# Kernel tuning notes

Hardware: AMD Instinct MI355X
Metric: run time of the kernel (lower is better)

Reference implementation:

```python
import jax, jax.numpy as jnp
import numpy as np

HID, QK_NOPE, QK_ROPE, Q_LR, KV_LR, H, V_DIM = 2048, 128, 64, 768, 512, 16, 128
QK_HEAD = QK_NOPE + QK_ROPE
THETA = 10000.0
EPS = 1e-5


def _layernorm(x, g, b):
    mu = jnp.mean(x, axis=-1, keepdims=True)
    var = jnp.mean(jnp.square(x - mu), axis=-1, keepdims=True)
    return (x - mu) * jax.lax.rsqrt(var + EPS) * g + b


def _rotate_half(x):
    x1, x2 = jnp.split(x, 2, axis=-1)
    return jnp.concatenate([-x2, x1], axis=-1)


def setup_inputs() -> dict:
    key = jax.random.key(0)
    ks = jax.random.split(key, 6)
    s = 0.02
    return {
        "hidden_state": jax.random.normal(ks[0], (2, 4096, HID), dtype=jnp.float32),
        "w_qa": jax.random.normal(ks[1], (Q_LR, HID), dtype=jnp.float32) * s,
        "b_qa": jnp.zeros((Q_LR,), jnp.float32),
        "g_qa_ln": jnp.ones((Q_LR,), jnp.float32),
        "b_qa_ln": jnp.zeros((Q_LR,), jnp.float32),
        "w_qb": jax.random.normal(ks[2], (H * QK_HEAD, Q_LR), dtype=jnp.float32) * s,
        "b_qb": jnp.zeros((H * QK_HEAD,), jnp.float32),
        "w_kva": jax.random.normal(ks[3], (KV_LR + QK_ROPE, HID), dtype=jnp.float32) * s,
        "b_kva": jnp.zeros((KV_LR + QK_ROPE,), jnp.float32),
        "g_kva_ln": jnp.ones((KV_LR,), jnp.float32),
        "b_kva_ln": jnp.zeros((KV_LR,), jnp.float32),
        "w_kvb": jax.random.normal(ks[4], (H * (QK_NOPE + V_DIM), KV_LR), dtype=jnp.float32) * s,
        "b_kvb": jnp.zeros((H * (QK_NOPE + V_DIM),), jnp.float32),
    }


def reference(hidden_state, w_qa, b_qa, g_qa_ln, b_qa_ln, w_qb, b_qb,
              w_kva, b_kva, g_kva_ln, b_kva_ln, w_kvb, b_kvb):
    B, S, _ = hidden_state.shape
    # ----- Q path: low-rank down-proj -> LN -> up-proj -----
    q_c = hidden_state @ w_qa.T + b_qa                      # [B,S,Q_LR]
    q_c = _layernorm(q_c, g_qa_ln, b_qa_ln)
    q = (q_c @ w_qb.T + b_qb).reshape(B, S, H, QK_HEAD).transpose(0, 2, 1, 3)  # [B,H,S,QK_HEAD]
    q_nope, q_rope = q[..., :QK_NOPE], q[..., QK_NOPE:]
    # ----- KV path -----
    kv_c = hidden_state @ w_kva.T + b_kva                   # [B,S,KV_LR+ROPE]
    kv_lr, k_rope = kv_c[..., :KV_LR], kv_c[..., KV_LR:]
    kv_lr = _layernorm(kv_lr, g_kva_ln, b_kva_ln)
    kv = (kv_lr @ w_kvb.T + b_kvb).reshape(B, S, H, QK_NOPE + V_DIM).transpose(0, 2, 1, 3)
    k_nope, v = kv[..., :QK_NOPE], kv[..., QK_NOPE:]
    # ----- RoPE on the rope slice only -----
    inv_freq = 1.0 / THETA ** (jnp.arange(0, QK_ROPE, 2, dtype=jnp.float32) / QK_ROPE)
    freq = jnp.arange(S, dtype=jnp.float32)[:, None] * inv_freq[None, :]   # [S, ROPE/2]
    cos = jnp.concatenate([jnp.cos(freq), jnp.cos(freq)], axis=-1)[None, None]  # [1,1,S,ROPE]
    sin = jnp.concatenate([jnp.sin(freq), jnp.sin(freq)], axis=-1)[None, None]
    k_rope = k_rope[:, None]                                # [B,1,S,ROPE]
    q_rot = q_rope * cos + _rotate_half(q_rope) * sin       # [B,H,S,ROPE]
    k_rot = k_rope * cos + _rotate_half(k_rope) * sin       # [B,1,S,ROPE]
    k_rot = jnp.broadcast_to(k_rot, (B, H, S, QK_ROPE))
    q_full = jnp.concatenate([q_nope, q_rot], axis=-1)      # [B,H,S,QK_HEAD]
    k_full = jnp.concatenate([k_nope, k_rot], axis=-1)      # [B,H,S,QK_HEAD]
    # original forward stops after building q,k,v; return them concatenated
    return jnp.concatenate([q_full, k_full, v], axis=-1)    # [B,H,S,2*QK_HEAD+V_DIM]
```

## Files before the change

kernel.cpp:

```cpp
#include <hip/hip_runtime.h>

typedef unsigned short u16;
typedef __bf16 bf16x8 __attribute__((ext_vector_type(8)));
typedef float f32x4 __attribute__((ext_vector_type(4)));

#define FENCE() asm volatile("" ::: "memory")
#define BARRIER()                      \
  do {                                 \
    FENCE();                           \
    __builtin_amdgcn_s_barrier();      \
    FENCE();                           \
  } while (0)


__device__ __forceinline__ u16 f2bf(float f) {
  unsigned u = __float_as_uint(f);
  u += 0x7fffu + ((u >> 16) & 1u);
  return (u16)(u >> 16);
}

__device__ __forceinline__ ushort4 f2bf4(float4 v) {
  return make_ushort4(f2bf(v.x), f2bf(v.y), f2bf(v.z), f2bf(v.w));
}

__device__ __forceinline__ void load_lds16(const void* g, void* l) {
  __builtin_amdgcn_global_load_lds(
      (const __attribute__((address_space(1))) void*)g,
      (__attribute__((address_space(3))) void*)l, 16, 0, 0);
}

__device__ __forceinline__ void conv_seg(const float* __restrict__ s,
                                         u16* __restrict__ d, int n4,
                                         int g, int stride) {
  const float4* s4 = (const float4*)s;
  ushort4* d4 = (ushort4*)d;
  for (int i = g; i < n4; i += stride) {
    float4 v = s4[i];
    d4[i] = make_ushort4(f2bf(v.x), f2bf(v.y), f2bf(v.z), f2bf(v.w));
  }
}


__global__ __launch_bounds__(256) void prep(
    const float* __restrict__ hid, const float* __restrict__ wqa,
    const float* __restrict__ wkva, const float* __restrict__ wqb,
    const float* __restrict__ wkvb, const float* __restrict__ bqa,
    const float* __restrict__ bkva, u16* __restrict__ hid_b,
    u16* __restrict__ wab_b, u16* __restrict__ wqb_b,
    u16* __restrict__ wkvb_b, float* __restrict__ bias_ab,
    float* __restrict__ cosT, float* __restrict__ sinT) {
  int g = blockIdx.x * 256 + threadIdx.x;
  int stride = gridDim.x * 256;
  conv_seg(hid, hid_b, 4194304, g, stride);
  conv_seg(wqa, wab_b, 393216, g, stride);
  conv_seg(wkva, wab_b + 768 * 2048, 294912, g, stride);
  conv_seg(wqb, wqb_b, 589824, g, stride);
  conv_seg(wkvb, wkvb_b, 524288, g, stride);
  if (g < 1344) bias_ab[g] = (g < 768) ? bqa[g] : bkva[g - 768];
  for (int idx = g; idx < 131072; idx += stride) {
    int s = idx >> 5, i = idx & 31;
    float inv = powf(10000.f, -(float)i / 32.f);
    float f = (float)s * inv;
    float sv, cv;
    sincosf(f, &sv, &cv);
    cosT[idx] = cv;
    sinT[idx] = sv;
  }
}


template <int WHICH>
__global__ __launch_bounds__(256, 2) void gemm_k(
    const u16* __restrict__ A0, const u16* __restrict__ B0,
    const float* __restrict__ bias0, float* __restrict__ C0,
    const u16* __restrict__ qA, const u16* __restrict__ qB,
    const float* __restrict__ qb, const u16* __restrict__ kA,
    const u16* __restrict__ kB, const float* __restrict__ kb,
    float* __restrict__ out, const float* __restrict__ cosT,
    const float* __restrict__ sinT) {
  __shared__ __align__(16) u16 smem[2 * 128 * 64];
  u16* sA = smem;
  u16* sB = smem + 128 * 64;
  const int tid = threadIdx.x;
  const int lane = tid & 63;
  const int wave = tid >> 6;
  const int wm = (wave >> 1) * 64;
  const int wn = (wave & 1) * 64;
  const int lane15 = lane & 15;
  const int quad = lane >> 4;
  const int mTile = blockIdx.x * 128;

  const u16* A;
  const u16* B;
  const float* bias;
  int K, nTile, mode;
  if (WHICH == 0) {
    A = A0; B = B0; bias = bias0; K = 2048; nTile = blockIdx.y * 128; mode = 0;
  } else if (blockIdx.y < 24) {
    A = qA; B = qB; bias = qb; K = 768; nTile = blockIdx.y * 128; mode = 1;
  } else {
    A = kA; B = kB; bias = kb; K = 512; nTile = (blockIdx.y - 24) * 128;
    mode = 2;
  }

  f32x4 acc[4][4] = {};

  const int nStages = K >> 6;
  for (int ks = 0; ks < nStages; ++ks) {
    const int k0 = ks << 6;
    if (ks) __syncthreads();
#pragma unroll
    for (int i = 0; i < 4; ++i) {
      int nu = i * 256 + tid;
      int rr = nu >> 3, u = nu & 7;
      int ul = u ^ (rr & 7);
      load_lds16(A + (size_t)(mTile + rr) * K + (k0 + ul * 8),
                 &sA[(i * 256 + (wave << 6)) * 8]);
    }
#pragma unroll
    for (int i = 0; i < 4; ++i) {
      int nu = i * 256 + tid;
      int rr = nu >> 3, u = nu & 7;
      int ul = u ^ (rr & 7);
      int brow = nTile + rr;
      if (WHICH == 0 && brow >= 1344) brow = 1343;
      load_lds16(B + (size_t)brow * K + (k0 + ul * 8),
                 &sB[(i * 256 + (wave << 6)) * 8]);
    }
    __syncthreads();
#pragma unroll
    for (int kk = 0; kk < 2; ++kk) {
      bf16x8 af[4], bfv[4];
#pragma unroll
      for (int mi = 0; mi < 4; ++mi) {
        int r = wm + mi * 16 + lane15;
        int u = (kk * 4 + quad) ^ (r & 7);
        af[mi] = *(const bf16x8*)&sA[(r * 8 + u) * 8];
      }
#pragma unroll
      for (int ni = 0; ni < 4; ++ni) {
        int r = wn + ni * 16 + lane15;
        int u = (kk * 4 + quad) ^ (r & 7);
        bfv[ni] = *(const bf16x8*)&sB[(r * 8 + u) * 8];
      }
#pragma unroll
      for (int mi = 0; mi < 4; ++mi)
#pragma unroll
        for (int ni = 0; ni < 4; ++ni)
          acc[mi][ni] = __builtin_amdgcn_mfma_f32_16x16x32_bf16(
              af[mi], bfv[ni], acc[mi][ni], 0, 0, 0);
    }
  }

  const int colW = nTile + wn;
  float bv[4];
#pragma unroll
  for (int ni = 0; ni < 4; ++ni) {
    int col = colW + ni * 16 + lane15;
    if (WHICH == 0)
      bv[ni] = (col < 1344) ? bias[col] : 0.f;
    else
      bv[ni] = bias[col];
  }

  int h = 0, ch0 = 0;
  if (mode == 1) {
    h = colW / 192;
    ch0 = colW % 192;
  } else if (mode == 2) {
    int jb = colW & 255;
    h = colW >> 8;
    ch0 = (jb < 128) ? (192 + jb) : (256 + jb);
  }
  const bool ropeTile = (mode == 1) && (ch0 == 128);

  __syncthreads();
  float* lw = (float*)smem + wave * (16 * 68);
  const int hi = lane15 >> 2, l3 = lane15 & 3;

#pragma unroll
  for (int mi = 0; mi < 4; ++mi) {
    f32x4 v[4];
#pragma unroll
    for (int ni = 0; ni < 4; ++ni)
#pragma unroll
      for (int rg = 0; rg < 4; ++rg) v[ni][rg] = acc[mi][ni][rg] + bv[ni];

    if (ropeTile) {
      int rowB = mTile + wm + mi * 16 + quad * 4;
#pragma unroll
      for (int rg = 0; rg < 4; ++rg) {
        int ss = (rowB + rg) & 4095;
#pragma unroll
        for (int ni = 0; ni < 2; ++ni) {
          int i = ni * 16 + lane15;
          float cv = cosT[ss * 32 + i], sv = sinT[ss * 32 + i];
          float x1 = v[ni][rg], x2 = v[ni + 2][rg];
          v[ni][rg] = x1 * cv - x2 * sv;
          v[ni + 2][rg] = x2 * cv + x1 * sv;
        }
      }
    }

    if (mi) asm volatile("s_waitcnt lgkmcnt(0)" ::: "memory");
#pragma unroll
    for (int ni = 0; ni < 4; ++ni) {
      int su = (4 * ni + hi) ^ quad;
#pragma unroll
      for (int rg = 0; rg < 4; ++rg)
        lw[68 * (quad * 4 + rg) + 4 * su + l3] = v[ni][rg];
    }
    asm volatile("s_waitcnt lgkmcnt(0)" ::: "memory");
#pragma unroll
    for (int j = 0; j < 4; ++j) {
      int rr = 4 * j + quad;
      int su = lane15 ^ j;
      float4 o = *(const float4*)&lw[68 * rr + 4 * su];
      int row = mTile + wm + mi * 16 + rr;
      if (mode == 0) {
        if (colW + 4 * lane15 < 1344)
          *(float4*)(C0 + (size_t)row * 1344 + colW + 4 * lane15) = o;
      } else {
        int bb = row >> 12, ss = row & 4095;
        size_t ob =
            ((size_t)((bb * 16 + h) * 4096 + ss)) * 512 + ch0 + 4 * lane15;
        *(float4*)(out + ob) = o;
      }
    }
  }
}

__global__ __launch_bounds__(512, 2) void gemm256(
    const u16* __restrict__ A, const u16* __restrict__ B,
    const float* __restrict__ bias, float* __restrict__ out) {
  __shared__ __align__(16) u16 smem[4 * 256 * 64];
  const int tid = threadIdx.x;
  const int lane = tid & 63;
  const int wave = tid >> 6;
  const int wm = (wave >> 2) * 128;
  const int wn = (wave & 3) * 64;
  const int lane15 = lane & 15;
  const int quad = lane >> 4;
  const int mTile = blockIdx.x * 256;
  const int nTile = blockIdx.y * 256;

  u16* const sA0 = smem;
  u16* const sB0 = smem + 2 * 16384;

#define STAGE8(kt, c)                                                         \
  do {                                                                        \
    u16* dA = sA0 + (c) * 16384;                                              \
    u16* dB = sB0 + (c) * 16384;                                              \
    _Pragma("unroll") for (int i = 0; i < 4; ++i) {                           \
      int g = i * 512 + tid;                                                  \
      int rr = g >> 3, ul = (g & 7) ^ (rr & 7);                               \
      load_lds16(A + (size_t)(mTile + rr) * 512 + (kt) * 64 + ul * 8,         \
                 dA + (i * 512 + (wave << 6)) * 8);                           \
    }                                                                         \
    _Pragma("unroll") for (int i = 0; i < 4; ++i) {                           \
      int g = i * 512 + tid;                                                  \
      int rr = g >> 3, ul = (g & 7) ^ (rr & 7);                               \
      load_lds16(B + (size_t)(nTile + rr) * 512 + (kt) * 64 + ul * 8,         \
                 dB + (i * 512 + (wave << 6)) * 8);                           \
    }                                                                         \
  } while (0)

  f32x4 acc[8][4] = {};

  STAGE8(0, 0);
  for (int t = 0; t < 8; ++t) {
    const int c = t & 1;
    const u16* sAc = sA0 + c * 16384;
    const u16* sBc = sB0 + c * 16384;
    if (t < 7) {
      STAGE8(t + 1, c ^ 1);
      asm volatile("s_waitcnt vmcnt(8)" ::: "memory");
    } else {
      asm volatile("s_waitcnt vmcnt(0)" ::: "memory");
    }
    BARRIER();
#pragma unroll
    for (int ph = 0; ph < 4; ++ph) {
      const int mh = ph >> 1, nh = ph & 1;
      bf16x8 af[4][2], bfv[2][2];
#pragma unroll
      for (int mi = 0; mi < 4; ++mi) {
        int r = wm + mh * 64 + mi * 16 + lane15;
#pragma unroll
        for (int kk = 0; kk < 2; ++kk) {
          int u = (kk * 4 + quad) ^ (r & 7);
          af[mi][kk] = *(const bf16x8*)&sAc[(r * 8 + u) * 8];
        }
      }
#pragma unroll
      for (int ni = 0; ni < 2; ++ni) {
        int rb = wn + nh * 32 + ni * 16 + lane15;
#pragma unroll
        for (int kk = 0; kk < 2; ++kk) {
          int u = (kk * 4 + quad) ^ (rb & 7);
          bfv[ni][kk] = *(const bf16x8*)&sBc[(rb * 8 + u) * 8];
        }
      }
      BARRIER();
      __builtin_amdgcn_s_setprio(1);
#pragma unroll
      for (int mi = 0; mi < 4; ++mi)
#pragma unroll
        for (int ni = 0; ni < 2; ++ni)
#pragma unroll
          for (int kk = 0; kk < 2; ++kk)
            acc[mh * 4 + mi][nh * 2 + ni] =
                __builtin_amdgcn_mfma_f32_16x16x32_bf16(
                    af[mi][kk], bfv[ni][kk], acc[mh * 4 + mi][nh * 2 + ni],
                    0, 0, 0);
      __builtin_amdgcn_s_setprio(0);
      BARRIER();
    }
  }
#undef STAGE8

  const int colW = nTile + wn;
  float bv[4];
#pragma unroll
  for (int ni = 0; ni < 4; ++ni) bv[ni] = bias[colW + ni * 16 + lane15];
  const int h = colW >> 8;
  const int jb = colW & 255;
  const int ch0 = (jb < 128) ? (192 + jb) : (256 + jb);

  float* lw = (float*)smem + wave * (16 * 68);
  const int hi = lane15 >> 2, l3 = lane15 & 3;

#pragma unroll
  for (int mi = 0; mi < 8; ++mi) {
    f32x4 v[4];
#pragma unroll
    for (int ni = 0; ni < 4; ++ni)
#pragma unroll
      for (int rg = 0; rg < 4; ++rg) v[ni][rg] = acc[mi][ni][rg] + bv[ni];

    if (mi) asm volatile("s_waitcnt lgkmcnt(0)" ::: "memory");
#pragma unroll
    for (int ni = 0; ni < 4; ++ni) {
      int su = (4 * ni + hi) ^ quad;
#pragma unroll
      for (int rg = 0; rg < 4; ++rg)
        lw[68 * (quad * 4 + rg) + 4 * su + l3] = v[ni][rg];
    }
    asm volatile("s_waitcnt lgkmcnt(0)" ::: "memory");
#pragma unroll
    for (int j = 0; j < 4; ++j) {
      int rr = 4 * j + quad;
      int su = lane15 ^ j;
      float4 o = *(const float4*)&lw[68 * rr + 4 * su];
      int row = mTile + wm + mi * 16 + rr;
      int bb = row >> 12, ss = row & 4095;
      size_t ob =
          ((size_t)((bb * 16 + h) * 4096 + ss)) * 512 + ch0 + 4 * lane15;
      *(float4*)(out + ob) = o;
    }
  }
}


__global__ __launch_bounds__(256) void ln_rot(
    const float* __restrict__ qkvc, const float* __restrict__ g_q,
    const float* __restrict__ b_q, const float* __restrict__ g_kv,
    const float* __restrict__ b_kv, u16* __restrict__ q_ln,
    u16* __restrict__ kv_ln, const float* __restrict__ cosT,
    const float* __restrict__ sinT, float* __restrict__ out) {
  __shared__ float red[4][4];
  __shared__ __align__(16) float rot[64];
  const int tid = threadIdx.x;
  const int t = blockIdx.x;
  const int bb = t >> 12, ss = t & 4095;
  const float4* p4 = (const float4*)(qkvc + (size_t)t * 1344);

  float4 a = p4[tid];
  float4 b = make_float4(0.f, 0.f, 0.f, 0.f);
  if (tid < 80) b = p4[256 + tid];

  float sa = a.x + a.y + a.z + a.w;
  float sqa = a.x * a.x + a.y * a.y + a.z * a.z + a.w * a.w;
  float qs = 0.f, qq = 0.f, ks = 0.f, kq = 0.f;
  if (tid < 192) { qs = sa; qq = sqa; } else { ks = sa; kq = sqa; }
  if (tid < 64) {
    ks += b.x + b.y + b.z + b.w;
    kq += b.x * b.x + b.y * b.y + b.z * b.z + b.w * b.w;
  }
#pragma unroll
  for (int off = 32; off > 0; off >>= 1) {
    qs += __shfl_down(qs, off, 64);
    qq += __shfl_down(qq, off, 64);
    ks += __shfl_down(ks, off, 64);
    kq += __shfl_down(kq, off, 64);
  }
  const int lane = tid & 63, wave = tid >> 6;
  if (lane == 0) {
    red[wave][0] = qs; red[wave][1] = qq;
    red[wave][2] = ks; red[wave][3] = kq;
  }
  __syncthreads();
  qs = red[0][0] + red[1][0] + red[2][0] + red[3][0];
  qq = red[0][1] + red[1][1] + red[2][1] + red[3][1];
  ks = red[0][2] + red[1][2] + red[2][2] + red[3][2];
  kq = red[0][3] + red[1][3] + red[2][3] + red[3][3];
  const float muq = qs * (1.f / 768.f);
  const float invq = rsqrtf(qq * (1.f / 768.f) - muq * muq + 1e-5f);
  const float muk = ks * (1.f / 512.f);
  const float invk = rsqrtf(kq * (1.f / 512.f) - muk * muk + 1e-5f);

  if (tid < 192) {
    float4 g = ((const float4*)g_q)[tid];
    float4 be = ((const float4*)b_q)[tid];
    float4 o = make_float4((a.x - muq) * invq * g.x + be.x,
                           (a.y - muq) * invq * g.y + be.y,
                           (a.z - muq) * invq * g.z + be.z,
                           (a.w - muq) * invq * g.w + be.w);
    ((ushort4*)(q_ln + (size_t)t * 768))[tid] = f2bf4(o);
  } else {
    int j = tid - 192;
    float4 g = ((const float4*)g_kv)[j];
    float4 be = ((const float4*)b_kv)[j];
    float4 o = make_float4((a.x - muk) * invk * g.x + be.x,
                           (a.y - muk) * invk * g.y + be.y,
                           (a.z - muk) * invk * g.z + be.z,
                           (a.w - muk) * invk * g.w + be.w);
    ((ushort4*)(kv_ln + (size_t)t * 512))[j] = f2bf4(o);
  }
  if (tid < 64) {
    int j = 64 + tid;
    float4 g = ((const float4*)g_kv)[j];
    float4 be = ((const float4*)b_kv)[j];
    float4 o = make_float4((b.x - muk) * invk * g.x + be.x,
                           (b.y - muk) * invk * g.y + be.y,
                           (b.z - muk) * invk * g.z + be.z,
                           (b.w - muk) * invk * g.w + be.w);
    ((ushort4*)(kv_ln + (size_t)t * 512))[j] = f2bf4(o);
  }
  if (tid < 32) {
    const float* p = qkvc + (size_t)t * 1344;
    float k1 = p[1280 + tid], k2 = p[1312 + tid];
    float cv = cosT[ss * 32 + tid], sv = sinT[ss * 32 + tid];
    rot[tid] = k1 * cv - k2 * sv;
    rot[tid + 32] = k2 * cv + k1 * sv;
  }
  __syncthreads();
  {
    int hh = tid >> 4, c4 = tid & 15;
    float4 o = ((const float4*)rot)[c4];
    *(float4*)(out + ((size_t)((bb * 16 + hh) * 4096 + ss)) * 512 + 320 +
               4 * c4) = o;
  }
}


extern "C" void kernel_launch(void* const* d_in, const int* in_sizes, int n_in,
                              void* d_out, int out_size, void* d_ws,
                              size_t ws_size, hipStream_t stream) {
  const float* hidden = (const float*)d_in[0];
  const float* w_qa = (const float*)d_in[1];
  const float* b_qa = (const float*)d_in[2];
  const float* g_qa_ln = (const float*)d_in[3];
  const float* b_qa_ln = (const float*)d_in[4];
  const float* w_qb = (const float*)d_in[5];
  const float* b_qb = (const float*)d_in[6];
  const float* w_kva = (const float*)d_in[7];
  const float* b_kva = (const float*)d_in[8];
  const float* g_kva_ln = (const float*)d_in[9];
  const float* b_kva_ln = (const float*)d_in[10];
  const float* w_kvb = (const float*)d_in[11];
  const float* b_kvb = (const float*)d_in[12];
  float* out = (float*)d_out;

  char* ws = (char*)d_ws;
  u16* hid_bf = (u16*)ws;   ws += (size_t)16777216 * 2;
  u16* wab_bf = (u16*)ws;   ws += (size_t)1344 * 2048 * 2;
  u16* wqb_bf = (u16*)ws;   ws += (size_t)2359296 * 2;
  u16* wkvb_bf = (u16*)ws;  ws += (size_t)2097152 * 2;
  float* qkvc = (float*)ws; ws += (size_t)8192 * 1344 * 4;
  u16* q_ln = (u16*)ws;     ws += (size_t)6291456 * 2;
  u16* kv_ln = (u16*)ws;    ws += (size_t)4194304 * 2;
  float* cosT = (float*)ws; ws += (size_t)131072 * 4;
  float* sinT = (float*)ws; ws += (size_t)131072 * 4;
  float* bias_ab = (float*)ws; ws += (size_t)2048 * 4;

  prep<<<dim3(1024), dim3(256), 0, stream>>>(
      hidden, w_qa, w_kva, w_qb, w_kvb, b_qa, b_kva, hid_bf, wab_bf, wqb_bf,
      wkvb_bf, bias_ab, cosT, sinT);
  gemm_k<0><<<dim3(64, 11), dim3(256), 0, stream>>>(
      hid_bf, wab_bf, bias_ab, qkvc, nullptr, nullptr, nullptr, nullptr,
      nullptr, nullptr, nullptr, cosT, sinT);
  ln_rot<<<dim3(8192), dim3(256), 0, stream>>>(qkvc, g_qa_ln, b_qa_ln,
                                               g_kva_ln, b_kva_ln, q_ln, kv_ln,
                                               cosT, sinT, out);
  gemm_k<1><<<dim3(64, 24), dim3(256), 0, stream>>>(
      nullptr, nullptr, nullptr, nullptr, q_ln, wqb_bf, b_qb, nullptr, nullptr,
      nullptr, out, cosT, sinT);
  gemm256<<<dim3(32, 16), dim3(512), 0, stream>>>(kv_ln, wkvb_bf, b_kvb, out);
}
```

Before: 480.3 us.

## Restructure KV up-projection GEMM into triple-buffered K=32 pipeline

The 256x256 KV GEMM now uses 16 k-steps of width 32 with a three-stage LDS ring instead of 8 steps of width 64 double-buffered. Loads for step j+2 are interleaved between the two MFMA halves, and each step has one barrier instead of eight barriers per tile. Shared memory drops to 96 KB and launch bounds allow one block per CU, trading occupancy for deeper prefetch and fewer synchronisations. The swizzle changes to match the narrower 4-chunk rows.

Result: slower. 490.8 us (+2.2%).

```diff
diff --git a/kernel.cpp b/kernel.cpp
--- a/kernel.cpp
+++ b/kernel.cpp
@@ -230,10 +230,10 @@
   }
 }
 
-__global__ __launch_bounds__(512, 2) void gemm256(
+__global__ __launch_bounds__(512, 1) void gemm256kv(
     const u16* __restrict__ A, const u16* __restrict__ B,
     const float* __restrict__ bias, float* __restrict__ out) {
-  __shared__ __align__(16) u16 smem[4 * 256 * 64];
+  __shared__ __align__(16) u16 smem[6 * 8192];
   const int tid = threadIdx.x;
   const int lane = tid & 63;
   const int wave = tid >> 6;
@@ -244,80 +244,77 @@
   const int mTile = blockIdx.x * 256;
   const int nTile = blockIdx.y * 256;
 
-  u16* const sA0 = smem;
-  u16* const sB0 = smem + 2 * 16384;
-
-#define STAGE8(kt, c)                                                         \
+#define STG(SRC, rowBase, kt, dstBase)                                        \
   do {                                                                        \
-    u16* dA = sA0 + (c) * 16384;                                              \
-    u16* dB = sB0 + (c) * 16384;                                              \
-    _Pragma("unroll") for (int i = 0; i < 4; ++i) {                           \
-      int g = i * 512 + tid;                                                  \
-      int rr = g >> 3, ul = (g & 7) ^ (rr & 7);                               \
-      load_lds16(A + (size_t)(mTile + rr) * 512 + (kt) * 64 + ul * 8,         \
-                 dA + (i * 512 + (wave << 6)) * 8);                           \
-    }                                                                         \
-    _Pragma("unroll") for (int i = 0; i < 4; ++i) {                           \
-      int g = i * 512 + tid;                                                  \
-      int rr = g >> 3, ul = (g & 7) ^ (rr & 7);                               \
-      load_lds16(B + (size_t)(nTile + rr) * 512 + (kt) * 64 + ul * 8,         \
-                 dB + (i * 512 + (wave << 6)) * 8);                           \
+    _Pragma("unroll") for (int l = 0; l < 2; ++l) {                           \
+      int g = l * 512 + tid;                                                  \
+      int rr = g >> 2;                                                        \
+      int ul = (g & 3) ^ ((rr >> 1) & 3);                                     \
+      load_lds16(SRC + (size_t)((rowBase) + rr) * 512 + (kt) * 32 + ul * 8,   \
+                 (dstBase) + (size_t)(l * 512 + (wave << 6)) * 8);            \
     }                                                                         \
   } while (0)
 
   f32x4 acc[8][4] = {};
 
-  STAGE8(0, 0);
-  for (int t = 0; t < 8; ++t) {
-    const int c = t & 1;
-    const u16* sAc = sA0 + c * 16384;
-    const u16* sBc = sB0 + c * 16384;
-    if (t < 7) {
-      STAGE8(t + 1, c ^ 1);
-      asm volatile("s_waitcnt vmcnt(8)" ::: "memory");
-    } else {
+  STG(A, mTile, 0, smem);
+  STG(B, nTile, 0, smem + 3 * 8192);
+  STG(A, mTile, 1, smem + 8192);
+  STG(B, nTile, 1, smem + 3 * 8192 + 8192);
+  asm volatile("s_waitcnt vmcnt(4)" ::: "memory");
+  BARRIER();
+
+  int s = 0;
+  for (int j = 0; j < 16; ++j) {
+    const u16* sAc = smem + s * 8192;
+    const u16* sBc = smem + (3 + s) * 8192;
+    int s2 = s + 2; if (s2 >= 3) s2 -= 3;
+
+    bf16x8 af[4], bfv[4];
+#pragma unroll
+    for (int mi = 0; mi < 4; ++mi) {
+      int r = wm + mi * 16 + lane15;
+      af[mi] = *(const bf16x8*)&sAc[(r * 4 + (quad ^ ((r >> 1) & 3))) * 8];
+    }
+#pragma unroll
+    for (int ni = 0; ni < 4; ++ni) {
+      int rb = wn + ni * 16 + lane15;
+      bfv[ni] = *(const bf16x8*)&sBc[(rb * 4 + (quad ^ ((rb >> 1) & 3))) * 8];
+    }
+    if (j < 14) STG(A, mTile, j + 2, smem + s2 * 8192);
+    __builtin_amdgcn_s_setprio(1);
+#pragma unroll
+    for (int mi = 0; mi < 4; ++mi)
+#pragma unroll
+      for (int ni = 0; ni < 4; ++ni)
+        acc[mi][ni] = __builtin_amdgcn_mfma_f32_16x16x32_bf16(
+            af[mi], bfv[ni], acc[mi][ni], 0, 0, 0);
+    __builtin_amdgcn_s_setprio(0);
+
+    bf16x8 af2[4];
+#pragma unroll
+    for (int mi = 0; mi < 4; ++mi) {
+      int r = wm + 64 + mi * 16 + lane15;
+      af2[mi] = *(const bf16x8*)&sAc[(r * 4 + (quad ^ ((r >> 1) & 3))) * 8];
+    }
+    if (j < 14) STG(B, nTile, j + 2, smem + (3 + s2) * 8192);
+    __builtin_amdgcn_s_setprio(1);
+#pragma unroll
+    for (int mi = 0; mi < 4; ++mi)
+#pragma unroll
+      for (int ni = 0; ni < 4; ++ni)
+        acc[4 + mi][ni] = __builtin_amdgcn_mfma_f32_16x16x32_bf16(
+            af2[mi], bfv[ni], acc[4 + mi][ni], 0, 0, 0);
+    __builtin_amdgcn_s_setprio(0);
+
+    if (j < 14)
+      asm volatile("s_waitcnt vmcnt(4)" ::: "memory");
+    else if (j == 14)
       asm volatile("s_waitcnt vmcnt(0)" ::: "memory");
-    }
     BARRIER();
-#pragma unroll
-    for (int ph = 0; ph < 4; ++ph) {
-      const int mh = ph >> 1, nh = ph & 1;
-      bf16x8 af[4][2], bfv[2][2];
-#pragma unroll
-      for (int mi = 0; mi < 4; ++mi) {
-        int r = wm + mh * 64 + mi * 16 + lane15;
-#pragma unroll
-        for (int kk = 0; kk < 2; ++kk) {
-          int u = (kk * 4 + quad) ^ (r & 7);
-          af[mi][kk] = *(const bf16x8*)&sAc[(r * 8 + u) * 8];
-        }
-      }
-#pragma unroll
-      for (int ni = 0; ni < 2; ++ni) {
-        int rb = wn + nh * 32 + ni * 16 + lane15;
-#pragma unroll
-        for (int kk = 0; kk < 2; ++kk) {
-          int u = (kk * 4 + quad) ^ (rb & 7);
-          bfv[ni][kk] = *(const bf16x8*)&sBc[(rb * 8 + u) * 8];
-        }
-      }
-      BARRIER();
-      __builtin_amdgcn_s_setprio(1);
-#pragma unroll
-      for (int mi = 0; mi < 4; ++mi)
-#pragma unroll
-        for (int ni = 0; ni < 2; ++ni)
-#pragma unroll
-          for (int kk = 0; kk < 2; ++kk)
-            acc[mh * 4 + mi][nh * 2 + ni] =
-                __builtin_amdgcn_mfma_f32_16x16x32_bf16(
-                    af[mi][kk], bfv[ni][kk], acc[mh * 4 + mi][nh * 2 + ni],
-                    0, 0, 0);
-      __builtin_amdgcn_s_setprio(0);
-      BARRIER();
-    }
-  }
-#undef STAGE8
+    s = (s == 2) ? 0 : s + 1;
+  }
+#undef STG
 
   const int colW = nTile + wn;
   float bv[4];
@@ -496,5 +493,6 @@
   gemm_k<1><<<dim3(64, 24), dim3(256), 0, stream>>>(
       nullptr, nullptr, nullptr, nullptr, q_ln, wqb_bf, b_qb, nullptr, nullptr,
       nullptr, out, cosT, sinT);
-  gemm256<<<dim3(32, 16), dim3(512), 0, stream>>>(kv_ln, wkvb_bf, b_kvb, out);
-}
+  gemm256kv<<<dim3(32, 16), dim3(512), 0, stream>>>(kv_ln, wkvb_bf, b_kvb,
+                                                    out);
+}
```
